# Optimization experiments

Hardware: AMD Instinct MI355X
Metric: run time of the kernel (lower is better)

The kernel has to match this reference:

```python
import jax, jax.numpy as jnp
import numpy as np

N_LAYERS, HEADS, D_IN, D_OUT, T, D, DFF = 4, 8, 16, 3, 1024, 512, 2048
D_HEAD = D // HEADS


def sinusoidal_pos_enc(t, d):
    # Faithful to the source: base = pos / 10000**(emb_idx/d); sin on even cols, cos on odd cols
    pos = jnp.arange(t, dtype=jnp.float32)[:, None]
    emb = jnp.arange(d, dtype=jnp.float32)[None, :]
    base = pos / jnp.power(10000.0, emb / d)
    even = (jnp.arange(d) % 2 == 0)[None, :]
    return jnp.where(even, jnp.sin(base), jnp.cos(base))  # (t, d)


def layer_norm(x, g, b, eps=1e-5):
    m = x.mean(-1, keepdims=True)
    v = ((x - m) ** 2).mean(-1, keepdims=True)
    return (x - m) / jnp.sqrt(v + eps) * g + b


def setup_inputs() -> dict:
    key = jax.random.key(0)
    ks = iter(jax.random.split(key, 24))
    s = 0.02
    inp = {}
    inp['x'] = jax.random.normal(next(ks), (16, T, D_IN), dtype=jnp.float32)
    inp['pad_mask'] = jax.random.randint(next(ks), (16, T), 0, 2, dtype=jnp.int32)
    inp['enc_W'] = jax.random.normal(next(ks), (D_IN, D), dtype=jnp.float32) * s
    inp['enc_b'] = jnp.zeros((D,), jnp.float32)
    for name in ['Wq', 'Wk', 'Wv', 'Wo']:
        inp[name] = jax.random.normal(next(ks), (N_LAYERS, D, D), dtype=jnp.float32) * s
    inp['ff_W1'] = jax.random.normal(next(ks), (N_LAYERS, D, DFF), dtype=jnp.float32) * s
    inp['ff_b1'] = jnp.zeros((N_LAYERS, DFF), jnp.float32)
    inp['ff_W2'] = jax.random.normal(next(ks), (N_LAYERS, DFF, D), dtype=jnp.float32) * s
    inp['ff_b2'] = jnp.zeros((N_LAYERS, D), jnp.float32)
    inp['ln1_g'] = jnp.ones((N_LAYERS, D), jnp.float32)
    inp['ln1_b'] = jnp.zeros((N_LAYERS, D), jnp.float32)
    inp['ln2_g'] = jnp.ones((N_LAYERS, D), jnp.float32)
    inp['ln2_b'] = jnp.zeros((N_LAYERS, D), jnp.float32)
    inp['out_W'] = jax.random.normal(next(ks), (D * T, D_OUT), dtype=jnp.float32) * s
    inp['out_b'] = jnp.zeros((D_OUT,), jnp.float32)
    return inp


def reference(x, enc_W, enc_b, Wq, Wk, Wv, Wo, ff_W1, ff_b1, ff_W2, ff_b2,
              ln1_g, ln1_b, ln2_g, ln2_b, out_W, out_b, pad_mask):
    n, t = x.shape[0], x.shape[1]
    # InputEncoding (linear) scaled by sqrt(d_model)
    h = (x @ enc_W + enc_b) * jnp.sqrt(jnp.float32(D))
    # Sinusoidal positional encoding, zeroed at masked (pad_mask==0) timesteps
    pe = sinusoidal_pos_enc(t, D)[None]  # (1, t, d)
    pe = jnp.where(pad_mask[..., None] == 0, 0.0, pe)  # (n, t, d)
    h = h + pe
    mask4 = (pad_mask[..., None, None] == 0)  # (n, t, 1, 1)
    for i in range(N_LAYERS):
        # --- MultiHeadAttention (faithful to source's transpose quirk) ---
        Qh = (h @ Wq[i]).reshape(n, t, HEADS, D_HEAD).swapaxes(2, 3)  # (n,t,dh,H)
        Kh = (h @ Wk[i]).reshape(n, t, HEADS, D_HEAD)                 # (n,t,H,dh)
        Vh = (h @ Wv[i]).reshape(n, t, HEADS, D_HEAD).swapaxes(2, 3)  # (n,t,dh,H)
        # energy: per-timestep (dh x dh), scaled by d_head**1/2 == d_head/2 (source precedence)
        energy = jnp.matmul(Qh, Kh) / (D_HEAD / 2.0)                  # (n,t,dh,dh)
        energy = jnp.where(mask4, -1e20, energy)
        attn = jax.nn.softmax(energy, axis=-1)
        head = jnp.matmul(attn, Vh)                                   # (n,t,dh,H)
        out = head.reshape(n, t, D) @ Wo[i]
        # residual + layer norm
        h = layer_norm(out + h, ln1_g[i], ln1_b[i])
        # --- FFN (relu) ---
        ff = jax.nn.relu(h @ ff_W1[i] + ff_b1[i]) @ ff_W2[i] + ff_b2[i]
        h = layer_norm(ff + h, ln2_g[i], ln2_b[i])
    # mode='train': flatten and project
    return h.reshape(n, -1) @ out_W + out_b  # (n, d_output)
```

## Files before the change

kernel.cpp:

```cpp
#include <hip/hip_runtime.h>
#include <cmath>

#define NB 16
#define TSEQ 1024
#define DIN 16
#define DM 512
#define DFFN 2048
#define NLAYERS 4
#define DOUTN 3
#define ROWS (NB*TSEQ)

typedef unsigned short u16;
typedef unsigned int   u32;
typedef short bf16x8 __attribute__((ext_vector_type(8)));
typedef u16   u16x4  __attribute__((ext_vector_type(4)));
typedef float f32x4  __attribute__((ext_vector_type(4)));

__device__ __forceinline__ float b2f(u16 v) { return __uint_as_float((unsigned)v << 16); }
__device__ __forceinline__ u16 f2b(float f) {
    unsigned u = __float_as_uint(f);
    return (u16)((u + 0x7FFFu + ((u >> 16) & 1u)) >> 16);
}

#define GLL(gp, lp) __builtin_amdgcn_global_load_lds( \
    (const __attribute__((address_space(1))) unsigned int*)(gp), \
    (__attribute__((address_space(3))) unsigned int*)(lp), 16, 0, 0)

template<int PERM>
__global__ __launch_bounds__(256) void transpose_cast(
    const float* __restrict__ in, u16* __restrict__ out,
    int K, int N, size_t in_lstride, size_t out_lstride)
{
    in  += (size_t)blockIdx.z * in_lstride;
    out += (size_t)blockIdx.z * out_lstride;
    __shared__ float t[32][33];
    int bk = blockIdx.x * 32, bn = blockIdx.y * 32;
    int x = threadIdx.x & 31, y = threadIdx.x >> 5;
    #pragma unroll
    for (int i = 0; i < 32; i += 8)
        t[y + i][x] = in[(size_t)(bk + y + i) * N + bn + x];
    __syncthreads();
    #pragma unroll
    for (int i = 0; i < 32; i += 8) {
        int row = bn + y + i;
        if (PERM) row = ((row & 63) << 3) | ((row >> 6) & 7);
        out[(size_t)row * K + bk + x] = f2b(t[x][y + i]);
    }
}

__global__ __launch_bounds__(128) void encode_kernel(
    const float* __restrict__ x, const int* __restrict__ pad,
    const float* __restrict__ W, const float* __restrict__ b,
    u16* __restrict__ h)
{
    int row = blockIdx.x;
    int t   = row & (TSEQ - 1);
    int c   = threadIdx.x * 4;
    float acc[4];
    #pragma unroll
    for (int j = 0; j < 4; ++j) acc[j] = b[c + j];
    const float* xr = x + (size_t)row * DIN;
    #pragma unroll
    for (int k = 0; k < DIN; ++k) {
        float xv = xr[k];
        const float* wr = W + (size_t)k * DM + c;
        #pragma unroll
        for (int j = 0; j < 4; ++j) acc[j] += xv * wr[j];
    }
    const float s = 22.62741699796952f;
    bool has_pe = (pad[row] != 0);
    u16x4 o;
    #pragma unroll
    for (int j = 0; j < 4; ++j) {
        acc[j] *= s;
        if (has_pe) {
            int d = c + j;
            float base = (float)t * powf(10000.0f, -(float)d * (1.0f/512.0f));
            acc[j] += ((d & 1) == 0) ? sinf(base) : cosf(base);
        }
        o[j] = f2b(acc[j]);
    }
    *(u16x4*)&h[(size_t)row * DM + c] = o;
}

template<int BIAS, int RELU>
__global__ __launch_bounds__(256) void gemm_bf16(
    const u16* __restrict__ A, const u16* __restrict__ Bt,
    const float* __restrict__ bias, u16* __restrict__ C,
    int M, int N, int K)
{
    __shared__ u16 As[128 * 64];
    __shared__ u16 Bs[128 * 64];
    const int tid  = threadIdx.x;
    const int lane = tid & 63;
    const int wid  = tid >> 6;
    const int wr   = wid >> 1, wc = wid & 1;
    const int bm   = blockIdx.x * 128;
    const int bn   = blockIdx.y * 128;

    const int srow8 = lane >> 3;
    const int sslot = lane & 7;
    const int scol  = ((sslot ^ srow8) * 8);
    const u16* Ag = A  + (size_t)(bm + wid * 32 + srow8) * K + scol;
    const u16* Bg = Bt + (size_t)(bn + wid * 32 + srow8) * K + scol;
    u16* Al = As + wid * 2048;
    u16* Bl = Bs + wid * 2048;

    f32x4 acc[4][4];
    #pragma unroll
    for (int m = 0; m < 4; ++m)
        #pragma unroll
        for (int n = 0; n < 4; ++n)
            acc[m][n] = (f32x4){0.f, 0.f, 0.f, 0.f};

    const int fr  = lane & 15;
    const int grp = lane >> 4;

    for (int k0 = 0; k0 < K; k0 += 64) {
        #pragma unroll
        for (int i = 0; i < 4; ++i) {
            GLL(Ag + (size_t)(i * 8) * K + k0, Al + i * 512);
            GLL(Bg + (size_t)(i * 8) * K + k0, Bl + i * 512);
        }
        __syncthreads();
        bf16x8 a[4][2];
        #pragma unroll
        for (int m = 0; m < 4; ++m) {
            int row = wr * 64 + m * 16 + fr;
            #pragma unroll
            for (int ks = 0; ks < 2; ++ks) {
                int slot = (ks * 4 + grp) ^ (row & 7);
                a[m][ks] = *(const bf16x8*)(As + row * 64 + slot * 8);
            }
        }
        #pragma unroll
        for (int n = 0; n < 4; ++n) {
            bf16x8 b[2];
            int row = wc * 64 + n * 16 + fr;
            #pragma unroll
            for (int ks = 0; ks < 2; ++ks) {
                int slot = (ks * 4 + grp) ^ (row & 7);
                b[ks] = *(const bf16x8*)(Bs + row * 64 + slot * 8);
            }
            #pragma unroll
            for (int m = 0; m < 4; ++m) {
                acc[m][n] = __builtin_amdgcn_mfma_f32_16x16x32_bf16(a[m][0], b[0], acc[m][n], 0, 0, 0);
                acc[m][n] = __builtin_amdgcn_mfma_f32_16x16x32_bf16(a[m][1], b[1], acc[m][n], 0, 0, 0);
            }
        }
        __syncthreads();
    }

    float bb[4] = {0.f, 0.f, 0.f, 0.f};
    if (BIAS) {
        #pragma unroll
        for (int n = 0; n < 4; ++n) bb[n] = bias[bn + wc * 64 + n * 16 + fr];
    }
    #pragma unroll
    for (int m = 0; m < 4; ++m) {
        #pragma unroll
        for (int n = 0; n < 4; ++n) {
            int col = bn + wc * 64 + n * 16 + fr;
            #pragma unroll
            for (int j = 0; j < 4; ++j) {
                int row = bm + wr * 64 + m * 16 + ((lane >> 4) << 2) + j;
                float v = acc[m][n][j];
                if (BIAS) v += bb[n];
                if (RELU) v = fmaxf(v, 0.f);
                C[(size_t)row * N + col] = f2b(v);
            }
        }
    }
}

__global__ __launch_bounds__(256) void attn_mfma(
    const u16* __restrict__ QKV, const int* __restrict__ pad,
    u16* __restrict__ O)
{
    constexpr int WLDS = 2560;
    __shared__ u16 sh[4 * WLDS];
    const int wid  = threadIdx.x >> 6;
    const int lane = threadIdx.x & 63;
    const int site = blockIdx.x * 4 + wid;
    u16* P2 = sh + wid * WLDS;
    u16* Ol = P2 + 2048;

    const u16* base = QKV + (size_t)site * 1536;
    const int fr  = lane & 15;
    const int grp = lane >> 4;
    const bf16x8 zb = {0,0,0,0,0,0,0,0};
    const f32x4  zf = {0.f,0.f,0.f,0.f};

    if (pad[site] == 0) {
        bf16x8 vv = *(const bf16x8*)(base + 1024 + lane * 8);
        float s = 0.f;
        #pragma unroll
        for (int j = 0; j < 8; ++j) s += b2f((u16)vv[j]);
        s += __shfl_xor(s, 1); s += __shfl_xor(s, 2); s += __shfl_xor(s, 4);
        s *= (1.0f / 64.0f);
        bf16x8 ov;
        #pragma unroll
        for (int h2 = 0; h2 < 8; ++h2) ov[h2] = (short)f2b(__shfl(s, h2 * 8));
        *(bf16x8*)(O + (size_t)site * DM + lane * 8) = ov;
        return;
    }

    bf16x8 kt[4];
    #pragma unroll
    for (int n = 0; n < 4; ++n)
        kt[n] = (grp == 0) ? *(const bf16x8*)(base + 512 + (n * 16 + fr) * 8) : zb;
    bf16x8 bv[2];
    #pragma unroll
    for (int ks = 0; ks < 2; ++ks)
        bv[ks] = (fr < 8) ? *(const bf16x8*)(base + 1024 + fr * 64 + ks * 32 + grp * 8) : zb;

    const int swz = (fr & 3) ^ (fr >> 2);
    u16x4 pk23[4][2];

    #pragma unroll
    for (int m = 0; m < 4; ++m) {
        bf16x8 aq = (grp == 0) ? *(const bf16x8*)(base + (m * 16 + fr) * 8) : zb;
        f32x4 ev[4];
        #pragma unroll
        for (int n = 0; n < 4; ++n)
            ev[n] = __builtin_amdgcn_mfma_f32_16x16x32_bf16(kt[n], aq, zf, 0, 0, 0);
        f32x4 t0, t1;
        #pragma unroll
        for (int j = 0; j < 4; ++j) { t0[j] = fmaxf(ev[0][j], ev[1][j]); t1[j] = fmaxf(ev[2][j], ev[3][j]); }
        float mx = -1e30f;
        #pragma unroll
        for (int j = 0; j < 4; ++j) mx = fmaxf(mx, fmaxf(t0[j], t1[j]));
        mx = fmaxf(mx, __shfl_xor(mx, 16));
        mx = fmaxf(mx, __shfl_xor(mx, 32));
        float p[4][4];
        float s = 0.f;
        #pragma unroll
        for (int n = 0; n < 4; ++n)
            #pragma unroll
            for (int j = 0; j < 4; ++j) {
                p[n][j] = __expf((ev[n][j] - mx) * 0.03125f);
                s += p[n][j];
            }
        s += __shfl_xor(s, 16);
        s += __shfl_xor(s, 32);
        float inv = 1.0f / s;
        u16x4 pk[4];
        #pragma unroll
        for (int n = 0; n < 4; ++n)
            #pragma unroll
            for (int j = 0; j < 4; ++j) pk[n][j] = f2b(p[n][j] * inv);
        int row = m * 16 + fr;
        #pragma unroll
        for (int n = 0; n < 2; ++n) {
            int chunk = (n * 2 + (grp >> 1)) ^ swz;
            *(u16x4*)(P2 + row * 32 + chunk * 8 + (grp & 1) * 4) = pk[n];
        }
        pk23[m][0] = pk[2];
        pk23[m][1] = pk[3];
    }

    f32x4 pv[4];
    #pragma unroll
    for (int m = 0; m < 4; ++m) {
        int row = m * 16 + fr;
        bf16x8 ap = *(const bf16x8*)(P2 + row * 32 + ((grp ^ swz) * 8));
        pv[m] = __builtin_amdgcn_mfma_f32_16x16x32_bf16(ap, bv[0], zf, 0, 0, 0);
    }
    asm volatile("s_waitcnt lgkmcnt(0)" ::: "memory");
    __builtin_amdgcn_sched_barrier(0);

    #pragma unroll
    for (int m = 0; m < 4; ++m) {
        int row = m * 16 + fr;
        #pragma unroll
        for (int n = 0; n < 2; ++n) {
            int chunk = (n * 2 + (grp >> 1)) ^ swz;
            *(u16x4*)(P2 + row * 32 + chunk * 8 + (grp & 1) * 4) = pk23[m][n];
        }
    }
    #pragma unroll
    for (int m = 0; m < 4; ++m) {
        int row = m * 16 + fr;
        bf16x8 ap = *(const bf16x8*)(P2 + row * 32 + ((grp ^ swz) * 8));
        pv[m] = __builtin_amdgcn_mfma_f32_16x16x32_bf16(ap, bv[1], pv[m], 0, 0, 0);
    }

    #pragma unroll
    for (int m = 0; m < 4; ++m)
        #pragma unroll
        for (int j = 0; j < 4; ++j) {
            int row = m * 16 + grp * 4 + j;
            if (fr < 8) Ol[row * 8 + fr] = f2b(pv[m][j]);
        }
    __syncthreads();
    bf16x8 o = *(const bf16x8*)(Ol + lane * 8);
    *(bf16x8*)(O + (size_t)site * DM + lane * 8) = o;
}

__global__ __launch_bounds__(256) void add_ln_kernel(
    const u16* __restrict__ A, u16* __restrict__ H,
    const float* __restrict__ g, const float* __restrict__ b)
{
    int row  = blockIdx.x * 4 + (threadIdx.x >> 6);
    int lane = threadIdx.x & 63;
    const u16* a = A + (size_t)row * DM + lane * 8;
    u16* h = H + (size_t)row * DM + lane * 8;
    bf16x8 av = *(const bf16x8*)a;
    bf16x8 hv = *(const bf16x8*)h;
    float v[8];
    float s = 0.f;
    #pragma unroll
    for (int j = 0; j < 8; ++j) { v[j] = b2f((u16)av[j]) + b2f((u16)hv[j]); s += v[j]; }
    #pragma unroll
    for (int off = 32; off > 0; off >>= 1) s += __shfl_xor(s, off, 64);
    float mean = s * (1.0f / 512.0f);
    float var = 0.f;
    #pragma unroll
    for (int j = 0; j < 8; ++j) { float d = v[j] - mean; var += d * d; }
    #pragma unroll
    for (int off = 32; off > 0; off >>= 1) var += __shfl_xor(var, off, 64);
    float rstd = rsqrtf(var * (1.0f / 512.0f) + 1e-5f);
    bf16x8 ov;
    #pragma unroll
    for (int j = 0; j < 8; ++j) {
        int d = lane * 8 + j;
        ov[j] = (short)f2b((v[j] - mean) * rstd * g[d] + b[d]);
    }
    *(bf16x8*)h = ov;
}

__global__ __launch_bounds__(256) void out_stage1(
    const u16* __restrict__ h, const float* __restrict__ W,
    float* __restrict__ partial)
{
    int b = blockIdx.x, s = blockIdx.y;
    int tid = threadIdx.x;
    const u16* hb = h + (size_t)b * (TSEQ * DM) + (size_t)s * 8192;
    const float* Wb = W + (size_t)s * 8192 * 3;
    float a0 = 0.f, a1 = 0.f, a2 = 0.f;
    #pragma unroll 4
    for (int it = 0; it < 32; ++it) {
        int i = it * 256 + tid;
        float hv = b2f(hb[i]);
        a0 += hv * Wb[i * 3 + 0];
        a1 += hv * Wb[i * 3 + 1];
        a2 += hv * Wb[i * 3 + 2];
    }
    __shared__ float red[3][256];
    red[0][tid] = a0; red[1][tid] = a1; red[2][tid] = a2;
    __syncthreads();
    for (int off = 128; off > 0; off >>= 1) {
        if (tid < off) {
            red[0][tid] += red[0][tid + off];
            red[1][tid] += red[1][tid + off];
            red[2][tid] += red[2][tid + off];
        }
        __syncthreads();
    }
    if (tid == 0) {
        partial[(b * 64 + s) * 3 + 0] = red[0][0];
        partial[(b * 64 + s) * 3 + 1] = red[1][0];
        partial[(b * 64 + s) * 3 + 2] = red[2][0];
    }
}

__global__ __launch_bounds__(64) void out_stage2(
    const float* __restrict__ partial, const float* __restrict__ ob,
    float* __restrict__ out)
{
    int t = threadIdx.x;
    if (t < NB * DOUTN) {
        int b = t / 3, o = t % 3;
        float s = ob[o];
        for (int k = 0; k < 64; ++k) s += partial[(b * 64 + k) * 3 + o];
        out[t] = s;
    }
}

extern "C" void kernel_launch(void* const* d_in, const int* in_sizes, int n_in,
                              void* d_out, int out_size, void* d_ws, size_t ws_size,
                              hipStream_t stream)
{
    const float* x    = (const float*)d_in[0];
    const int*   pad  = (const int*)  d_in[1];
    const float* encW = (const float*)d_in[2];
    const float* encB = (const float*)d_in[3];
    const float* Wq   = (const float*)d_in[4];
    const float* Wk   = (const float*)d_in[5];
    const float* Wv   = (const float*)d_in[6];
    const float* Wo   = (const float*)d_in[7];
    const float* fW1  = (const float*)d_in[8];
    const float* fb1  = (const float*)d_in[9];
    const float* fW2  = (const float*)d_in[10];
    const float* fb2  = (const float*)d_in[11];
    const float* l1g  = (const float*)d_in[12];
    const float* l1b  = (const float*)d_in[13];
    const float* l2g  = (const float*)d_in[14];
    const float* l2b  = (const float*)d_in[15];
    const float* outW = (const float*)d_in[16];
    const float* outB = (const float*)d_in[17];
    float* out = (float*)d_out;

    const size_t WL  = 3145728;
    const size_t BUF = (size_t)ROWS * DM;
    const size_t need = (4 * WL + 6 * BUF) * sizeof(u16);
    if (ws_size < need) return;
    u16* wt = (u16*)d_ws;
    u16* h  = wt + 4 * WL;
    u16* b0 = h  + BUF;
    u16* b3 = b0 + 3 * BUF;
    u16* b4 = b3 + BUF;

    transpose_cast<1><<<dim3(16,16,4), 256, 0, stream>>>(Wq,  wt + 0,       512,  512,  (size_t)512*512,  WL);
    transpose_cast<1><<<dim3(16,16,4), 256, 0, stream>>>(Wk,  wt + 262144,  512,  512,  (size_t)512*512,  WL);
    transpose_cast<0><<<dim3(16,16,4), 256, 0, stream>>>(Wv,  wt + 524288,  512,  512,  (size_t)512*512,  WL);
    transpose_cast<0><<<dim3(16,16,4), 256, 0, stream>>>(Wo,  wt + 786432,  512,  512,  (size_t)512*512,  WL);
    transpose_cast<0><<<dim3(16,64,4), 256, 0, stream>>>(fW1, wt + 1048576, 512,  2048, (size_t)512*2048, WL);
    transpose_cast<0><<<dim3(64,16,4), 256, 0, stream>>>(fW2, wt + 2097152, 2048, 512,  (size_t)2048*512, WL);

    encode_kernel<<<ROWS, 128, 0, stream>>>(x, pad, encW, encB, h);

    for (int l = 0; l < NLAYERS; ++l) {
        u16* wl = wt + (size_t)l * WL;
        gemm_bf16<0,0><<<dim3(128,12), 256, 0, stream>>>(h, wl, nullptr, b0, ROWS, 1536, DM);
        attn_mfma<<<ROWS/4, 256, 0, stream>>>(b0, pad, b3);
        gemm_bf16<0,0><<<dim3(128,4), 256, 0, stream>>>(b3, wl + 786432, nullptr, b4, ROWS, DM, DM);
        add_ln_kernel<<<ROWS/4, 256, 0, stream>>>(b4, h, l1g + l*DM, l1b + l*DM);
        gemm_bf16<1,1><<<dim3(128,16), 256, 0, stream>>>(h, wl + 1048576, fb1 + (size_t)l*DFFN, b0, ROWS, DFFN, DM);
        gemm_bf16<1,0><<<dim3(128,4),  256, 0, stream>>>(b0, wl + 2097152, fb2 + (size_t)l*DM, b4, ROWS, DM, DFFN);
        add_ln_kernel<<<ROWS/4, 256, 0, stream>>>(b4, h, l2g + l*DM, l2b + l*DM);
    }

    out_stage1<<<dim3(NB, 64), 256, 0, stream>>>(h, outW, (float*)b0);
    out_stage2<<<1, 64, 0, stream>>>((float*)b0, outB, out);
}
```

Baseline: 781.6 us.

## Double-buffer A tile in LDS, load B directly from global, swizzle block order

```diff
diff --git a/kernel.cpp b/kernel.cpp
--- a/kernel.cpp
+++ b/kernel.cpp
@@ -89,22 +89,24 @@
     const float* __restrict__ bias, u16* __restrict__ C,
     int M, int N, int K)
 {
-    __shared__ u16 As[128 * 64];
-    __shared__ u16 Bs[128 * 64];
+    __shared__ u16 S[2][8192];
     const int tid  = threadIdx.x;
     const int lane = tid & 63;
     const int wid  = tid >> 6;
     const int wr   = wid >> 1, wc = wid & 1;
-    const int bm   = blockIdx.x * 128;
-    const int bn   = blockIdx.y * 128;
+
+    const int NY  = N >> 7;
+    const int nwg = gridDim.x;
+    const int cpx = nwg >> 3;
+    const int bid = blockIdx.x;
+    const int swz = (bid & 7) * cpx + (bid >> 3);
+    const int bm  = (swz / NY) * 128;
+    const int bn  = (swz % NY) * 128;
 
     const int srow8 = lane >> 3;
     const int sslot = lane & 7;
     const int scol  = ((sslot ^ srow8) * 8);
-    const u16* Ag = A  + (size_t)(bm + wid * 32 + srow8) * K + scol;
-    const u16* Bg = Bt + (size_t)(bn + wid * 32 + srow8) * K + scol;
-    u16* Al = As + wid * 2048;
-    u16* Bl = Bs + wid * 2048;
+    const u16* Ag = A + (size_t)(bm + wid * 32 + srow8) * K + scol;
 
     f32x4 acc[4][4];
     #pragma unroll
@@ -115,14 +117,28 @@
 
     const int fr  = lane & 15;
     const int grp = lane >> 4;
-
+    const u16* Bg = Bt + (size_t)(bn + wc * 64 + fr) * K + grp * 8;
+
+    auto STAGEA = [&](int k0, int d) {
+        u16* Al = S[d] + wid * 2048;
+        #pragma unroll
+        for (int i = 0; i < 4; ++i)
+            GLL(Ag + (size_t)(i * 8) * K + k0, Al + i * 512);
+    };
+
+    STAGEA(0, 0);
+    __syncthreads();
+
+    int cur = 0;
     for (int k0 = 0; k0 < K; k0 += 64) {
-        #pragma unroll
-        for (int i = 0; i < 4; ++i) {
-            GLL(Ag + (size_t)(i * 8) * K + k0, Al + i * 512);
-            GLL(Bg + (size_t)(i * 8) * K + k0, Bl + i * 512);
-        }
-        __syncthreads();
+        if (k0 + 64 < K) STAGEA(k0 + 64, cur ^ 1);
+        const u16* As = S[cur];
+        bf16x8 b[4][2];
+        #pragma unroll
+        for (int n = 0; n < 4; ++n)
+            #pragma unroll
+            for (int ks = 0; ks < 2; ++ks)
+                b[n][ks] = *(const bf16x8*)(Bg + (size_t)(n * 16) * K + k0 + ks * 32);
         bf16x8 a[4][2];
         #pragma unroll
         for (int m = 0; m < 4; ++m) {
@@ -134,21 +150,14 @@
             }
         }
         #pragma unroll
-        for (int n = 0; n < 4; ++n) {
-            bf16x8 b[2];
-            int row = wc * 64 + n * 16 + fr;
-            #pragma unroll
-            for (int ks = 0; ks < 2; ++ks) {
-                int slot = (ks * 4 + grp) ^ (row & 7);
-                b[ks] = *(const bf16x8*)(Bs + row * 64 + slot * 8);
+        for (int n = 0; n < 4; ++n)
+            #pragma unroll
+            for (int m = 0; m < 4; ++m) {
+                acc[m][n] = __builtin_amdgcn_mfma_f32_16x16x32_bf16(a[m][0], b[n][0], acc[m][n], 0, 0, 0);
+                acc[m][n] = __builtin_amdgcn_mfma_f32_16x16x32_bf16(a[m][1], b[n][1], acc[m][n], 0, 0, 0);
             }
-            #pragma unroll
-            for (int m = 0; m < 4; ++m) {
-                acc[m][n] = __builtin_amdgcn_mfma_f32_16x16x32_bf16(a[m][0], b[0], acc[m][n], 0, 0, 0);
-                acc[m][n] = __builtin_amdgcn_mfma_f32_16x16x32_bf16(a[m][1], b[1], acc[m][n], 0, 0, 0);
-            }
-        }
         __syncthreads();
+        cur ^= 1;
     }
 
     float bb[4] = {0.f, 0.f, 0.f, 0.f};
@@ -422,12 +431,12 @@
 
     for (int l = 0; l < NLAYERS; ++l) {
         u16* wl = wt + (size_t)l * WL;
-        gemm_bf16<0,0><<<dim3(128,12), 256, 0, stream>>>(h, wl, nullptr, b0, ROWS, 1536, DM);
+        gemm_bf16<0,0><<<dim3((ROWS/128)*(1536/128)), 256, 0, stream>>>(h, wl, nullptr, b0, ROWS, 1536, DM);
         attn_mfma<<<ROWS/4, 256, 0, stream>>>(b0, pad, b3);
-        gemm_bf16<0,0><<<dim3(128,4), 256, 0, stream>>>(b3, wl + 786432, nullptr, b4, ROWS, DM, DM);
+        gemm_bf16<0,0><<<dim3((ROWS/128)*(DM/128)), 256, 0, stream>>>(b3, wl + 786432, nullptr, b4, ROWS, DM, DM);
         add_ln_kernel<<<ROWS/4, 256, 0, stream>>>(b4, h, l1g + l*DM, l1b + l*DM);
-        gemm_bf16<1,1><<<dim3(128,16), 256, 0, stream>>>(h, wl + 1048576, fb1 + (size_t)l*DFFN, b0, ROWS, DFFN, DM);
-        gemm_bf16<1,0><<<dim3(128,4),  256, 0, stream>>>(b0, wl + 2097152, fb2 + (size_t)l*DM, b4, ROWS, DM, DFFN);
+        gemm_bf16<1,1><<<dim3((ROWS/128)*(DFFN/128)), 256, 0, stream>>>(h, wl + 1048576, fb1 + (size_t)l*DFFN, b0, ROWS, DFFN, DM);
+        gemm_bf16<1,0><<<dim3((ROWS/128)*(DM/128)), 256, 0, stream>>>(b0, wl + 2097152, fb2 + (size_t)l*DM, b4, ROWS, DM, DFFN);
         add_ln_kernel<<<ROWS/4, 256, 0, stream>>>(b4, h, l2g + l*DM, l2b + l*DM);
     }
 
```

Measured after the change: 1.198 ms. 1.53x slower.
